# Kernel optimization log

Measured on AMD Instinct MI355X. Metric: run time of the kernel, lower is better.

The kernel has to match this reference:

```python
import jax, jax.numpy as jnp
import numpy as np

E = 2048   # embedding_size
H = 2048   # hidden_size
B = 512    # batch
OUT = 2    # output_size (coords)


def setup_inputs() -> dict:
    key = jax.random.key(0)
    ks = jax.random.split(key, 11)
    s = 0.02
    return {
        "embedding": jax.random.normal(ks[0], (B, E), dtype=jnp.float32),
        "max_seq_length": 256,
        "W_embed": jax.random.normal(ks[1], (H, E), dtype=jnp.float32) * s,
        "b_embed": jnp.zeros((H,), dtype=jnp.float32),
        "W_ih": jax.random.normal(ks[2], (4 * H, OUT), dtype=jnp.float32) * s,
        "b_ih": jnp.zeros((4 * H,), dtype=jnp.float32),
        "W_hh": jax.random.normal(ks[3], (4 * H, H), dtype=jnp.float32) * s,
        "b_hh": jnp.zeros((4 * H,), dtype=jnp.float32),
        "W_out": jax.random.normal(ks[4], (OUT, H), dtype=jnp.float32) * s,
        "b_out": jnp.zeros((OUT,), dtype=jnp.float32),
        "W_stop": jax.random.normal(ks[5], (1, H), dtype=jnp.float32) * s,
        "b_stop": jnp.zeros((1,), dtype=jnp.float32),
    }


def reference(embedding, max_seq_length, W_embed, b_embed, W_ih, b_ih,
              W_hh, b_hh, W_out, b_out, W_stop, b_stop):
    # h_0 from embedding head (num_layers == 1)
    h0 = embedding @ W_embed.T + b_embed          # (B, H)
    c0 = jnp.zeros_like(h0)
    x0 = jnp.zeros((embedding.shape[0], OUT), dtype=embedding.dtype)

    def step(carry, _):
        h, c, x = carry
        gates = x @ W_ih.T + b_ih + h @ W_hh.T + b_hh    # (B, 4H)
        i, f, g, o = jnp.split(gates, 4, axis=-1)         # torch gate order i,f,g,o
        c = jax.nn.sigmoid(f) * c + jax.nn.sigmoid(i) * jnp.tanh(g)
        h = jax.nn.sigmoid(o) * jnp.tanh(c)
        coord = h @ W_out.T + b_out                        # (B, 2)
        stop = jax.nn.sigmoid(h @ W_stop.T + b_stop)       # (B, 1)
        return (h, c, coord), (coord, stop)

    _, (coords, stops) = jax.lax.scan(step, (h0, c0, x0), xs=None,
                                      length=max_seq_length)
    outputs = jnp.transpose(coords, (1, 0, 2))     # (B, T, 2)
    stop_probs = jnp.transpose(stops, (1, 0, 2))   # (B, T, 1)
    return outputs, stop_probs
```

## Files before the change

kernel.cpp:

```cpp
#include <hip/hip_runtime.h>
#include <stdint.h>

#define E_DIM 2048
#define H_DIM 2048
#define B_DIM 512
#define T_DIM 256
#define G4H   8192

typedef unsigned short u16;
typedef __attribute__((ext_vector_type(8))) short bf16x8;
typedef __attribute__((ext_vector_type(4))) float f32x4;

__device__ inline u16 f2b(float f) {
  union { float f; uint32_t i; } v; v.f = f;
  uint32_t u = v.i;
  return (u16)((u + 0x7FFFu + ((u >> 16) & 1u)) >> 16);
}
__device__ inline float b2f(u16 u) {
  union { uint32_t i; float f; } v; v.i = ((uint32_t)u) << 16; return v.f;
}

__global__ __launch_bounds__(256) void convert_bf16(const float* __restrict__ s,
                                                    u16* __restrict__ d, int n4) {
  int i = blockIdx.x * 256 + threadIdx.x;
  if (i < n4) {
    float4 f = ((const float4*)s)[i];
    ushort4 o;
    o.x = f2b(f.x); o.y = f2b(f.y); o.z = f2b(f.z); o.w = f2b(f.w);
    ((ushort4*)d)[i] = o;
  }
}

__global__ __launch_bounds__(256) void build_weff(const float* __restrict__ W,
                                                  const float* __restrict__ W_ih,
                                                  const float* __restrict__ W_out,
                                                  u16* __restrict__ Wz) {
  int id = blockIdx.x * 256 + threadIdx.x;
  int lane = id & 63;
  int k32  = (id >> 6) & 63;
  int n16  = id >> 12;
  int np = n16 * 16 + (lane & 15);
  int k  = k32 * 32 + (lane >> 4) * 8;
  int g = np & 3, jrow = np >> 2;
  int src = g * H_DIM + jrow;
  float wi0 = W_ih[src * 2 + 0], wi1 = W_ih[src * 2 + 1];
  const float* sw = W + (size_t)src * H_DIM + k;
  u16 out[8];
  for (int j = 0; j < 8; ++j) {
    float v = sw[j] + wi0 * W_out[k + j] + wi1 * W_out[H_DIM + k + j];
    out[j] = f2b(v);
  }
  u16* dst = Wz + (size_t)id * 8;
  *(ushort4*)(dst) = *(ushort4*)&out[0];
  *(ushort4*)(dst + 4) = *(ushort4*)&out[4];
}

__global__ __launch_bounds__(256) void build_epi(const float* __restrict__ b_ih,
                                                 const float* __restrict__ b_hh,
                                                 const float* __restrict__ W_ih,
                                                 const float* __restrict__ b_out,
                                                 float* __restrict__ epi) {
  int np = blockIdx.x * 256 + threadIdx.x;
  int src = (np & 3) * H_DIM + (np >> 2);
  float wi0 = W_ih[src * 2 + 0], wi1 = W_ih[src * 2 + 1];
  float4 e;
  e.x = b_ih[src] + b_hh[src] + b_out[0] * wi0 + b_out[1] * wi1;
  e.y = wi0;
  e.z = wi1;
  e.w = 0.f;
  ((float4*)epi)[np] = e;
}

#define BM 64
#define BN 128
#define BK 32
__global__ __launch_bounds__(256) void gemm_bt(const u16* __restrict__ A,
                                               const u16* __restrict__ Bm,
                                               float* __restrict__ C,
                                               int M, int N, int K) {
  __shared__ u16 sA[BM * BK];
  __shared__ u16 sB[BN * BK];
  const int t = threadIdx.x;
  const int bm0 = blockIdx.y * BM, bn0 = blockIdx.x * BN;
  const int wave = t >> 6, lane = t & 63;
  const int wm = (wave >> 1) * 32, wn = (wave & 1) * 64;
  const int r16 = lane & 15, quad = lane >> 4;

  f32x4 acc[2][4];
  const f32x4 z = {0.f, 0.f, 0.f, 0.f};
  for (int i = 0; i < 2; ++i)
    for (int j = 0; j < 4; ++j) acc[i][j] = z;

  const int arow = t >> 2, acg = t & 3;

  for (int k0 = 0; k0 < K; k0 += BK) {
    __syncthreads();
    *(uint4*)&sA[arow * BK + acg * 8] =
        *(const uint4*)&A[(size_t)(bm0 + arow) * K + k0 + acg * 8];
    for (int i = 0; i < 2; ++i) {
      int c = t + 256 * i;
      int row = c >> 2, cg = c & 3;
      *(uint4*)&sB[row * BK + cg * 8] =
          *(const uint4*)&Bm[(size_t)(bn0 + row) * K + k0 + cg * 8];
    }
    __syncthreads();
    bf16x8 af[2], bfr[4];
    for (int mt = 0; mt < 2; ++mt)
      af[mt] = *(const bf16x8*)&sA[(wm + mt * 16 + r16) * BK + quad * 8];
    for (int nt = 0; nt < 4; ++nt)
      bfr[nt] = *(const bf16x8*)&sB[(wn + nt * 16 + r16) * BK + quad * 8];
    for (int mt = 0; mt < 2; ++mt)
      for (int nt = 0; nt < 4; ++nt)
        acc[mt][nt] = __builtin_amdgcn_mfma_f32_16x16x32_bf16(af[mt], bfr[nt],
                                                              acc[mt][nt], 0, 0, 0);
  }
  for (int mt = 0; mt < 2; ++mt)
    for (int nt = 0; nt < 4; ++nt) {
      int row = bm0 + wm + mt * 16 + quad * 4;
      int col = bn0 + wn + nt * 16 + r16;
      for (int r = 0; r < 4; ++r)
        C[(size_t)(row + r) * N + col] = acc[mt][nt][r];
    }
}

__global__ __launch_bounds__(256) void init_state(const float* __restrict__ h0pre,
                                                  const float* __restrict__ b_embed,
                                                  u16* __restrict__ h,
                                                  float* __restrict__ c,
                                                  float* __restrict__ xzero) {
  int idx = blockIdx.x * 256 + threadIdx.x;
  int bg = idx >> 11, k = idx & (H_DIM - 1);
  float v = h0pre[idx] + b_embed[k];
  size_t chunk = (((size_t)(bg >> 4)) * 64 + (k >> 5)) * 64 + ((k >> 3) & 3) * 16 + (bg & 15);
  size_t pos = chunk * 8 + (k & 7);
  h[pos] = f2b(v);
  c[pos] = 0.f;
  if (idx < B_DIM * 2) xzero[idx] = 0.f;
}

__global__ __launch_bounds__(64) void calc_xcorr(const float* __restrict__ h0pre,
                                                 const float* __restrict__ b_embed,
                                                 const float* __restrict__ W_out,
                                                 const float* __restrict__ b_out,
                                                 float* __restrict__ xc) {
  int m = blockIdx.x, ln = threadIdx.x;
  float s0 = 0.f, s1 = 0.f;
  for (int k = ln; k < H_DIM; k += 64) {
    float hv = h0pre[(size_t)m * H_DIM + k] + b_embed[k];
    s0 += hv * W_out[k];
    s1 += hv * W_out[H_DIM + k];
  }
  for (int off = 32; off > 0; off >>= 1) {
    s0 += __shfl_down(s0, off);
    s1 += __shfl_down(s1, off);
  }
  if (ln == 0) {
    xc[m * 2 + 0] = -(s0 + b_out[0]);
    xc[m * 2 + 1] = -(s1 + b_out[1]);
  }
}

__global__ __launch_bounds__(256) void init_out(const float* __restrict__ b_out,
                                                const float* __restrict__ b_stop,
                                                float* __restrict__ coords,
                                                float* __restrict__ stops) {
  int i = blockIdx.x * 256 + threadIdx.x;
  coords[i * 2 + 0] = b_out[0];
  coords[i * 2 + 1] = b_out[1];
  stops[i] = b_stop[0];
}

__global__ __launch_bounds__(256) void finalize_stops(float* __restrict__ stops) {
  int i = blockIdx.x * 256 + threadIdx.x;
  stops[i] = 1.f / (1.f + __expf(-stops[i]));
}

__global__ __launch_bounds__(512) void gemm_lstm(const u16* __restrict__ hA,
                                                 const u16* __restrict__ Wz,
                                                 const float* __restrict__ epi,
                                                 const float* __restrict__ x,
                                                 float* __restrict__ c,
                                                 u16* __restrict__ h_out,
                                                 const float* __restrict__ W_out,
                                                 const float* __restrict__ W_stop,
                                                 float* __restrict__ coords,
                                                 float* __restrict__ stops,
                                                 int trow) {
  __shared__ char smem[131072];
  float* cb = (float*)smem;
  float* gt = (float*)smem;

  const int bid = blockIdx.x;
  const int nt = (bid & 7) * 8 + ((bid >> 3) & 7);
  const int mt = bid >> 6;
  const int bm0 = mt * 128;

  const int t = threadIdx.x, wv = t >> 6, ln = t & 63;
  const int wn2 = wv & 1, kq = wv >> 1;
  const int r16 = ln & 15, quad = ln >> 4;

  const u16* pA[8];
  const u16* pB[4];
  for (int i = 0; i < 8; ++i)
    pA[i] = hA + (size_t)((bm0 >> 4) + i) * 32768 + (size_t)(kq * 16) * 512 + ln * 8;
  for (int i = 0; i < 4; ++i)
    pB[i] = Wz + (size_t)(nt * 8 + wn2 * 4 + i) * 32768 + (size_t)(kq * 16) * 512 + ln * 8;

  f32x4 acc[8][4];
  const f32x4 z = {0.f, 0.f, 0.f, 0.f};
  for (int i = 0; i < 8; ++i)
    for (int j = 0; j < 4; ++j) acc[i][j] = z;

  bf16x8 af[2][8], bf[2][4];
  for (int i = 0; i < 8; ++i) af[0][i] = *(const bf16x8*)(pA[i]);
  for (int i = 0; i < 4; ++i) bf[0][i] = *(const bf16x8*)(pB[i]);

#pragma unroll 2
  for (int kk = 0; kk < 16; ++kk) {
    const int cu = kk & 1;
    if (kk < 15) {
      const int nx = cu ^ 1;
      const size_t off = (size_t)(kk + 1) * 512;
      for (int i = 0; i < 8; ++i) af[nx][i] = *(const bf16x8*)(pA[i] + off);
      for (int i = 0; i < 4; ++i) bf[nx][i] = *(const bf16x8*)(pB[i] + off);
    }
    for (int mi = 0; mi < 8; ++mi)
      for (int ni = 0; ni < 4; ++ni)
        acc[mi][ni] = __builtin_amdgcn_mfma_f32_16x16x32_bf16(af[cu][mi], bf[cu][ni],
                                                              acc[mi][ni], 0, 0, 0);
  }

  if (kq >= 2) {
    float* dst = cb + ((kq - 2) * 2 + wn2) * 8192;
    for (int mi = 0; mi < 8; ++mi)
      for (int ni = 0; ni < 4; ++ni)
        *(f32x4*)&dst[((mi * 4 + ni) * 64 + ln) * 4] = acc[mi][ni];
  }
  __syncthreads();
  if (kq < 2) {
    const float* src = cb + (kq * 2 + wn2) * 8192;
    for (int mi = 0; mi < 8; ++mi)
      for (int ni = 0; ni < 4; ++ni)
        acc[mi][ni] += *(const f32x4*)&src[((mi * 4 + ni) * 64 + ln) * 4];
  }
  __syncthreads();
  if (kq == 1) {
    float* dst = cb + wn2 * 8192;
    for (int mi = 0; mi < 8; ++mi)
      for (int ni = 0; ni < 4; ++ni)
        *(f32x4*)&dst[((mi * 4 + ni) * 64 + ln) * 4] = acc[mi][ni];
  }
  __syncthreads();
  if (kq == 0) {
    const float* src = cb + wn2 * 8192;
    for (int mi = 0; mi < 8; ++mi)
      for (int ni = 0; ni < 4; ++ni)
        acc[mi][ni] += *(const f32x4*)&src[((mi * 4 + ni) * 64 + ln) * 4];
  }

  for (int half = 0; half < 2; ++half) {
    __syncthreads();
    if (wv < 2) {
      for (int mi = 0; mi < 4; ++mi)
        for (int ni = 0; ni < 4; ++ni) {
          int row = mi * 16 + quad * 4;
          int col = wn2 * 64 + ni * 16 + r16;
          f32x4 v = acc[half * 4 + mi][ni];
          for (int r = 0; r < 4; ++r)
            gt[(row + r) * 132 + col] = v[r];
        }
    }
    __syncthreads();
    if ((wv >> 2) == half) {
      const int q = wv & 3;
      const int lrow = q * 16 + r16;
      const int bg = bm0 + half * 64 + lrow;
      const float x0 = x[bg * 2 + 0], x1 = x[bg * 2 + 1];
      const size_t chunk = (((size_t)(bg >> 4)) * 64 + nt) * 64 + ln;
      const int hc0 = nt * 32 + quad * 8;
      float cv[8]; u16 hv[8];
      float s0 = 0.f, s1 = 0.f, s2 = 0.f;
      const float4* epi4 = (const float4*)epi;
      for (int j = 0; j < 8; ++j) {
        int col = quad * 32 + j * 4;
        float4 g4 = *(const float4*)&gt[lrow * 132 + col];
        float4 e0 = epi4[nt * 128 + col + 0];
        float4 e1 = epi4[nt * 128 + col + 1];
        float4 e2 = epi4[nt * 128 + col + 2];
        float4 e3 = epi4[nt * 128 + col + 3];
        float gi = g4.x + e0.x + x0 * e0.y + x1 * e0.z;
        float gf = g4.y + e1.x + x0 * e1.y + x1 * e1.z;
        float gg = g4.z + e2.x + x0 * e2.y + x1 * e2.z;
        float go = g4.w + e3.x + x0 * e3.y + x1 * e3.z;
        float si = 1.f / (1.f + __expf(-gi));
        float sf = 1.f / (1.f + __expf(-gf));
        float so = 1.f / (1.f + __expf(-go));
        float cn = sf * c[chunk * 8 + j] + si * tanhf(gg);
        cv[j] = cn;
        float hf = so * tanhf(cn);
        hv[j] = f2b(hf);
        s0 += hf * W_out[hc0 + j];
        s1 += hf * W_out[H_DIM + hc0 + j];
        s2 += hf * W_stop[hc0 + j];
      }
      *(float4*)&c[chunk * 8 + 0] = *(float4*)&cv[0];
      *(float4*)&c[chunk * 8 + 4] = *(float4*)&cv[4];
      *(ushort4*)&h_out[chunk * 8 + 0] = *(ushort4*)&hv[0];
      *(ushort4*)&h_out[chunk * 8 + 4] = *(ushort4*)&hv[4];
      s0 += __shfl_xor(s0, 16); s1 += __shfl_xor(s1, 16); s2 += __shfl_xor(s2, 16);
      s0 += __shfl_xor(s0, 32); s1 += __shfl_xor(s1, 32); s2 += __shfl_xor(s2, 32);
      if (quad == 0) {
        atomicAdd(&coords[((size_t)bg * T_DIM + trow) * 2 + 0], s0);
        atomicAdd(&coords[((size_t)bg * T_DIM + trow) * 2 + 1], s1);
        atomicAdd(&stops[(size_t)bg * T_DIM + trow], s2);
      }
    }
  }
}

extern "C" void kernel_launch(void* const* d_in, const int* in_sizes, int n_in,
                              void* d_out, int out_size, void* d_ws, size_t ws_size,
                              hipStream_t stream) {
  const float* embedding = (const float*)d_in[0];
  const float* W_embed   = (const float*)d_in[2];
  const float* b_embed   = (const float*)d_in[3];
  const float* W_ih      = (const float*)d_in[4];
  const float* b_ih      = (const float*)d_in[5];
  const float* W_hh      = (const float*)d_in[6];
  const float* b_hh      = (const float*)d_in[7];
  const float* W_out     = (const float*)d_in[8];
  const float* b_out     = (const float*)d_in[9];
  const float* W_stop    = (const float*)d_in[10];
  const float* b_stop    = (const float*)d_in[11];

  float* coords = (float*)d_out;
  float* stops  = (float*)d_out + (size_t)B_DIM * T_DIM * 2;

  char* ws = (char*)d_ws;
  u16* W_z     = (u16*)ws;   ws += (size_t)G4H * H_DIM * 2;
  u16* W_emb_b = (u16*)ws;   ws += (size_t)H_DIM * E_DIM * 2;
  u16* emb_b   = (u16*)ws;   ws += (size_t)B_DIM * E_DIM * 2;
  float* h0pre = (float*)ws; ws += (size_t)B_DIM * H_DIM * 4;
  float* epi   = (float*)ws; ws += (size_t)G4H * 4 * 4;
  float* cbuf  = (float*)ws; ws += (size_t)B_DIM * H_DIM * 4;
  u16* hbuf0   = (u16*)ws;   ws += (size_t)B_DIM * H_DIM * 2;
  u16* hbuf1   = (u16*)ws;   ws += (size_t)B_DIM * H_DIM * 2;
  float* xcorr = (float*)ws; ws += (size_t)B_DIM * 2 * 4;
  float* xzero = (float*)ws; ws += (size_t)B_DIM * 2 * 4;

  convert_bf16<<<(B_DIM * E_DIM / 4 + 255) / 256, 256, 0, stream>>>(embedding, emb_b, B_DIM * E_DIM / 4);
  convert_bf16<<<(H_DIM * E_DIM / 4 + 255) / 256, 256, 0, stream>>>(W_embed, W_emb_b, H_DIM * E_DIM / 4);
  build_weff<<<(G4H * H_DIM / 8) / 256, 256, 0, stream>>>(W_hh, W_ih, W_out, W_z);
  build_epi<<<G4H / 256, 256, 0, stream>>>(b_ih, b_hh, W_ih, b_out, epi);
  init_out<<<(B_DIM * T_DIM) / 256, 256, 0, stream>>>(b_out, b_stop, coords, stops);

  gemm_bt<<<dim3(H_DIM / BN, B_DIM / BM), 256, 0, stream>>>(emb_b, W_emb_b, h0pre,
                                                            B_DIM, H_DIM, E_DIM);
  init_state<<<(B_DIM * H_DIM) / 256, 256, 0, stream>>>(h0pre, b_embed, hbuf0, cbuf, xzero);
  calc_xcorr<<<B_DIM, 64, 0, stream>>>(h0pre, b_embed, W_out, b_out, xcorr);

  for (int t = 0; t < T_DIM; ++t) {
    u16* h_in  = (t & 1) ? hbuf1 : hbuf0;
    u16* h_out = (t & 1) ? hbuf0 : hbuf1;
    const float* xv = (t == 0) ? xcorr : xzero;
    gemm_lstm<<<256, 512, 0, stream>>>(h_in, W_z, epi, xv, cbuf, h_out,
                                       W_out, W_stop, coords, stops, t);
  }
  finalize_stops<<<(B_DIM * T_DIM) / 256, 256, 0, stream>>>(stops);
}
```

Measured before the change: 7.818 ms.

## Switch recurrent GEMM to 32x32x16 MFMA with matching pre-swizzled layouts

Replaces the 16x16x32 bf16 MFMA tiles with 32x32x16 MFMA tiles in the per-step gate GEMM. The weight, hidden-state and cell-state swizzled layouts (build_weff, init_state and the epilogue addressing) are changed to 32-row by 16-k chunks to match. The larger instruction cuts the number of MFMA issues and the operand loads per FLOP in the recurrent kernel. In exchange, the accumulator-to-shared scatter becomes more complex and all layout index math has to stay consistent across kernels.

```diff
diff --git a/kernel.cpp b/kernel.cpp
--- a/kernel.cpp
+++ b/kernel.cpp
@@ -10,6 +10,7 @@
 typedef unsigned short u16;
 typedef __attribute__((ext_vector_type(8))) short bf16x8;
 typedef __attribute__((ext_vector_type(4))) float f32x4;
+typedef __attribute__((ext_vector_type(16))) float f32x16;
 
 __device__ inline u16 f2b(float f) {
   union { float f; uint32_t i; } v; v.f = f;
@@ -37,10 +38,10 @@
                                                   u16* __restrict__ Wz) {
   int id = blockIdx.x * 256 + threadIdx.x;
   int lane = id & 63;
-  int k32  = (id >> 6) & 63;
-  int n16  = id >> 12;
-  int np = n16 * 16 + (lane & 15);
-  int k  = k32 * 32 + (lane >> 4) * 8;
+  int k16  = (id >> 6) & 127;
+  int n32  = id >> 13;
+  int np = n32 * 32 + (lane & 31);
+  int k  = k16 * 16 + (lane >> 5) * 8;
   int g = np & 3, jrow = np >> 2;
   int src = g * H_DIM + jrow;
   float wi0 = W_ih[src * 2 + 0], wi1 = W_ih[src * 2 + 1];
@@ -131,7 +132,7 @@
   int idx = blockIdx.x * 256 + threadIdx.x;
   int bg = idx >> 11, k = idx & (H_DIM - 1);
   float v = h0pre[idx] + b_embed[k];
-  size_t chunk = (((size_t)(bg >> 4)) * 64 + (k >> 5)) * 64 + ((k >> 3) & 3) * 16 + (bg & 15);
+  size_t chunk = (((size_t)(bg >> 5)) * 128 + (k >> 4)) * 64 + ((k >> 3) & 1) * 32 + (bg & 31);
   size_t pos = chunk * 8 + (k & 7);
   h[pos] = f2b(v);
   c[pos] = 0.f;
@@ -199,76 +200,93 @@
   const int wn2 = wv & 1, kq = wv >> 1;
   const int r16 = ln & 15, quad = ln >> 4;
 
-  const u16* pA[8];
-  const u16* pB[4];
-  for (int i = 0; i < 8; ++i)
-    pA[i] = hA + (size_t)((bm0 >> 4) + i) * 32768 + (size_t)(kq * 16) * 512 + ln * 8;
+  const u16* pA[4];
+  const u16* pB[2];
   for (int i = 0; i < 4; ++i)
-    pB[i] = Wz + (size_t)(nt * 8 + wn2 * 4 + i) * 32768 + (size_t)(kq * 16) * 512 + ln * 8;
-
-  f32x4 acc[8][4];
-  const f32x4 z = {0.f, 0.f, 0.f, 0.f};
-  for (int i = 0; i < 8; ++i)
-    for (int j = 0; j < 4; ++j) acc[i][j] = z;
-
-  bf16x8 af[2][8], bf[2][4];
-  for (int i = 0; i < 8; ++i) af[0][i] = *(const bf16x8*)(pA[i]);
-  for (int i = 0; i < 4; ++i) bf[0][i] = *(const bf16x8*)(pB[i]);
+    pA[i] = hA + ((size_t)(mt * 4 + i) * 128 + kq * 32) * 512 + ln * 8;
+  for (int i = 0; i < 2; ++i)
+    pB[i] = Wz + ((size_t)(nt * 4 + wn2 * 2 + i) * 128 + kq * 32) * 512 + ln * 8;
+
+  f32x16 acc[4][2];
+  for (int i = 0; i < 4; ++i)
+    for (int j = 0; j < 2; ++j)
+      for (int r = 0; r < 16; ++r) acc[i][j][r] = 0.f;
+
+  bf16x8 af[2][4], bf[2][2];
+  for (int i = 0; i < 4; ++i) af[0][i] = *(const bf16x8*)(pA[i]);
+  for (int i = 0; i < 2; ++i) bf[0][i] = *(const bf16x8*)(pB[i]);
 
 #pragma unroll 2
-  for (int kk = 0; kk < 16; ++kk) {
+  for (int kk = 0; kk < 32; ++kk) {
     const int cu = kk & 1;
-    if (kk < 15) {
+    if (kk < 31) {
       const int nx = cu ^ 1;
       const size_t off = (size_t)(kk + 1) * 512;
-      for (int i = 0; i < 8; ++i) af[nx][i] = *(const bf16x8*)(pA[i] + off);
-      for (int i = 0; i < 4; ++i) bf[nx][i] = *(const bf16x8*)(pB[i] + off);
-    }
-    for (int mi = 0; mi < 8; ++mi)
-      for (int ni = 0; ni < 4; ++ni)
-        acc[mi][ni] = __builtin_amdgcn_mfma_f32_16x16x32_bf16(af[cu][mi], bf[cu][ni],
+      for (int i = 0; i < 4; ++i) af[nx][i] = *(const bf16x8*)(pA[i] + off);
+      for (int i = 0; i < 2; ++i) bf[nx][i] = *(const bf16x8*)(pB[i] + off);
+    }
+    for (int mi = 0; mi < 4; ++mi)
+      for (int ni = 0; ni < 2; ++ni)
+        acc[mi][ni] = __builtin_amdgcn_mfma_f32_32x32x16_bf16(af[cu][mi], bf[cu][ni],
                                                               acc[mi][ni], 0, 0, 0);
   }
 
   if (kq >= 2) {
     float* dst = cb + ((kq - 2) * 2 + wn2) * 8192;
-    for (int mi = 0; mi < 8; ++mi)
-      for (int ni = 0; ni < 4; ++ni)
-        *(f32x4*)&dst[((mi * 4 + ni) * 64 + ln) * 4] = acc[mi][ni];
+    for (int mi = 0; mi < 4; ++mi)
+      for (int ni = 0; ni < 2; ++ni)
+        for (int q4 = 0; q4 < 4; ++q4) {
+          f32x4 v = {acc[mi][ni][q4 * 4 + 0], acc[mi][ni][q4 * 4 + 1],
+                     acc[mi][ni][q4 * 4 + 2], acc[mi][ni][q4 * 4 + 3]};
+          *(f32x4*)&dst[(((mi * 2 + ni) * 4 + q4) * 64 + ln) * 4] = v;
+        }
   }
   __syncthreads();
   if (kq < 2) {
     const float* src = cb + (kq * 2 + wn2) * 8192;
-    for (int mi = 0; mi < 8; ++mi)
-      for (int ni = 0; ni < 4; ++ni)
-        acc[mi][ni] += *(const f32x4*)&src[((mi * 4 + ni) * 64 + ln) * 4];
+    for (int mi = 0; mi < 4; ++mi)
+      for (int ni = 0; ni < 2; ++ni)
+        for (int q4 = 0; q4 < 4; ++q4) {
+          f32x4 p = *(const f32x4*)&src[(((mi * 2 + ni) * 4 + q4) * 64 + ln) * 4];
+          for (int e = 0; e < 4; ++e) acc[mi][ni][q4 * 4 + e] += p[e];
+        }
   }
   __syncthreads();
   if (kq == 1) {
     float* dst = cb + wn2 * 8192;
-    for (int mi = 0; mi < 8; ++mi)
-      for (int ni = 0; ni < 4; ++ni)
-        *(f32x4*)&dst[((mi * 4 + ni) * 64 + ln) * 4] = acc[mi][ni];
+    for (int mi = 0; mi < 4; ++mi)
+      for (int ni = 0; ni < 2; ++ni)
+        for (int q4 = 0; q4 < 4; ++q4) {
+          f32x4 v = {acc[mi][ni][q4 * 4 + 0], acc[mi][ni][q4 * 4 + 1],
+                     acc[mi][ni][q4 * 4 + 2], acc[mi][ni][q4 * 4 + 3]};
+          *(f32x4*)&dst[(((mi * 2 + ni) * 4 + q4) * 64 + ln) * 4] = v;
+        }
   }
   __syncthreads();
   if (kq == 0) {
     const float* src = cb + wn2 * 8192;
-    for (int mi = 0; mi < 8; ++mi)
-      for (int ni = 0; ni < 4; ++ni)
-        acc[mi][ni] += *(const f32x4*)&src[((mi * 4 + ni) * 64 + ln) * 4];
+    for (int mi = 0; mi < 4; ++mi)
+      for (int ni = 0; ni < 2; ++ni)
+        for (int q4 = 0; q4 < 4; ++q4) {
+          f32x4 p = *(const f32x4*)&src[(((mi * 2 + ni) * 4 + q4) * 64 + ln) * 4];
+          for (int e = 0; e < 4; ++e) acc[mi][ni][q4 * 4 + e] += p[e];
+        }
   }
 
   for (int half = 0; half < 2; ++half) {
     __syncthreads();
     if (wv < 2) {
-      for (int mi = 0; mi < 4; ++mi)
-        for (int ni = 0; ni < 4; ++ni) {
-          int row = mi * 16 + quad * 4;
-          int col = wn2 * 64 + ni * 16 + r16;
-          f32x4 v = acc[half * 4 + mi][ni];
-          for (int r = 0; r < 4; ++r)
-            gt[(row + r) * 132 + col] = v[r];
-        }
+      for (int mi2 = 0; mi2 < 2; ++mi2) {
+        int mi = half * 2 + mi2;
+        for (int ni = 0; ni < 2; ++ni) {
+          int col = wn2 * 64 + ni * 32 + (ln & 31);
+          int rbase = mi2 * 32 + 4 * (ln >> 5);
+          for (int r = 0; r < 16; ++r) {
+            int row = rbase + (r & 3) + 8 * (r >> 2);
+            gt[row * 132 + col] = acc[mi][ni][r];
+          }
+        }
+      }
     }
     __syncthreads();
     if ((wv >> 2) == half) {
@@ -276,8 +294,9 @@
       const int lrow = q * 16 + r16;
       const int bg = bm0 + half * 64 + lrow;
       const float x0 = x[bg * 2 + 0], x1 = x[bg * 2 + 1];
-      const size_t chunk = (((size_t)(bg >> 4)) * 64 + nt) * 64 + ln;
       const int hc0 = nt * 32 + quad * 8;
+      const size_t pos = (((size_t)(bg >> 5)) * 128 + (hc0 >> 4)) * 512 +
+                         ((hc0 >> 3) & 1) * 256 + (bg & 31) * 8;
       float cv[8]; u16 hv[8];
       float s0 = 0.f, s1 = 0.f, s2 = 0.f;
       const float4* epi4 = (const float4*)epi;
@@ -295,7 +314,7 @@
         float si = 1.f / (1.f + __expf(-gi));
         float sf = 1.f / (1.f + __expf(-gf));
         float so = 1.f / (1.f + __expf(-go));
-        float cn = sf * c[chunk * 8 + j] + si * tanhf(gg);
+        float cn = sf * c[pos + j] + si * tanhf(gg);
         cv[j] = cn;
         float hf = so * tanhf(cn);
         hv[j] = f2b(hf);
@@ -303,10 +322,10 @@
         s1 += hf * W_out[H_DIM + hc0 + j];
         s2 += hf * W_stop[hc0 + j];
       }
-      *(float4*)&c[chunk * 8 + 0] = *(float4*)&cv[0];
-      *(float4*)&c[chunk * 8 + 4] = *(float4*)&cv[4];
-      *(ushort4*)&h_out[chunk * 8 + 0] = *(ushort4*)&hv[0];
-      *(ushort4*)&h_out[chunk * 8 + 4] = *(ushort4*)&hv[4];
+      *(float4*)&c[pos + 0] = *(float4*)&cv[0];
+      *(float4*)&c[pos + 4] = *(float4*)&cv[4];
+      *(ushort4*)&h_out[pos + 0] = *(ushort4*)&hv[0];
+      *(ushort4*)&h_out[pos + 4] = *(ushort4*)&hv[4];
       s0 += __shfl_xor(s0, 16); s1 += __shfl_xor(s1, 16); s2 += __shfl_xor(s2, 16);
       s0 += __shfl_xor(s0, 32); s1 += __shfl_xor(s1, 32); s2 += __shfl_xor(s2, 32);
       if (quad == 0) {
```

Result: slower. 8.484 ms (+8.5%).

## Halve LSTM step M-tile to 64 rows and launch 512 blocks

Applied to the files above, without the earlier changes.

The per-step fused GEMM+LSTM kernel now uses 64-row batch tiles instead of 128, doubling the grid to 512 blocks. Shared memory is halved and launch bounds request 4 blocks per CU, so occupancy and CU coverage on the 256-CU device rise. The explicit register double-buffering of A/B fragments is dropped for a simple unroll-1 load-then-MFMA loop. In exchange each block re-reads the weight tile with half the batch reuse, which doubles weight traffic from L2, and the loop no longer overlaps loads with MFMAs in software.

```diff
diff --git a/kernel.cpp b/kernel.cpp
--- a/kernel.cpp
+++ b/kernel.cpp
@@ -175,145 +175,133 @@
   stops[i] = 1.f / (1.f + __expf(-stops[i]));
 }
 
-__global__ __launch_bounds__(512) void gemm_lstm(const u16* __restrict__ hA,
-                                                 const u16* __restrict__ Wz,
-                                                 const float* __restrict__ epi,
-                                                 const float* __restrict__ x,
-                                                 float* __restrict__ c,
-                                                 u16* __restrict__ h_out,
-                                                 const float* __restrict__ W_out,
-                                                 const float* __restrict__ W_stop,
-                                                 float* __restrict__ coords,
-                                                 float* __restrict__ stops,
-                                                 int trow) {
-  __shared__ char smem[131072];
+__global__ __launch_bounds__(512, 4) void gemm_lstm(const u16* __restrict__ hA,
+                                                    const u16* __restrict__ Wz,
+                                                    const float* __restrict__ epi,
+                                                    const float* __restrict__ x,
+                                                    float* __restrict__ c,
+                                                    u16* __restrict__ h_out,
+                                                    const float* __restrict__ W_out,
+                                                    const float* __restrict__ W_stop,
+                                                    float* __restrict__ coords,
+                                                    float* __restrict__ stops,
+                                                    int trow) {
+  __shared__ char smem[65536];
   float* cb = (float*)smem;
   float* gt = (float*)smem;
 
   const int bid = blockIdx.x;
   const int nt = (bid & 7) * 8 + ((bid >> 3) & 7);
   const int mt = bid >> 6;
-  const int bm0 = mt * 128;
+  const int bm0 = mt * 64;
 
   const int t = threadIdx.x, wv = t >> 6, ln = t & 63;
-  const int wn2 = wv & 1, kq = wv >> 1;
+  const int nh = wv & 1, kq = wv >> 1;
   const int r16 = ln & 15, quad = ln >> 4;
 
-  const u16* pA[8];
-  const u16* pB[4];
-  for (int i = 0; i < 8; ++i)
-    pA[i] = hA + (size_t)((bm0 >> 4) + i) * 32768 + (size_t)(kq * 16) * 512 + ln * 8;
+  const u16* pA = hA + ((size_t)(mt * 4) * 64 + (size_t)(kq * 16)) * 512 + ln * 8;
+  const u16* pB = Wz + ((size_t)(nt * 8 + nh * 4) * 64 + (size_t)(kq * 16)) * 512 + ln * 8;
+
+  f32x4 acc[4][4];
+  const f32x4 z = {0.f, 0.f, 0.f, 0.f};
   for (int i = 0; i < 4; ++i)
-    pB[i] = Wz + (size_t)(nt * 8 + wn2 * 4 + i) * 32768 + (size_t)(kq * 16) * 512 + ln * 8;
-
-  f32x4 acc[8][4];
-  const f32x4 z = {0.f, 0.f, 0.f, 0.f};
-  for (int i = 0; i < 8; ++i)
     for (int j = 0; j < 4; ++j) acc[i][j] = z;
 
-  bf16x8 af[2][8], bf[2][4];
-  for (int i = 0; i < 8; ++i) af[0][i] = *(const bf16x8*)(pA[i]);
-  for (int i = 0; i < 4; ++i) bf[0][i] = *(const bf16x8*)(pB[i]);
-
-#pragma unroll 2
+#pragma unroll 1
   for (int kk = 0; kk < 16; ++kk) {
-    const int cu = kk & 1;
-    if (kk < 15) {
-      const int nx = cu ^ 1;
-      const size_t off = (size_t)(kk + 1) * 512;
-      for (int i = 0; i < 8; ++i) af[nx][i] = *(const bf16x8*)(pA[i] + off);
-      for (int i = 0; i < 4; ++i) bf[nx][i] = *(const bf16x8*)(pB[i] + off);
+    bf16x8 af[4], bf[4];
+    for (int i = 0; i < 4; ++i) af[i] = *(const bf16x8*)(pA + (size_t)i * 32768);
+    for (int i = 0; i < 4; ++i) bf[i] = *(const bf16x8*)(pB + (size_t)i * 32768);
+    for (int mi = 0; mi < 4; ++mi)
+      for (int ni = 0; ni < 4; ++ni)
+        acc[mi][ni] = __builtin_amdgcn_mfma_f32_16x16x32_bf16(af[mi], bf[ni],
+                                                              acc[mi][ni], 0, 0, 0);
+    pA += 512;
+    pB += 512;
+  }
+
+  if (kq >= 2) {
+    float* dst = cb + ((kq - 2) * 2 + nh) * 4096;
+    for (int mi = 0; mi < 4; ++mi)
+      for (int ni = 0; ni < 4; ++ni)
+        *(f32x4*)&dst[((mi * 4 + ni) * 64 + ln) * 4] = acc[mi][ni];
+  }
+  __syncthreads();
+  if (kq < 2) {
+    const float* src = cb + (kq * 2 + nh) * 4096;
+    for (int mi = 0; mi < 4; ++mi)
+      for (int ni = 0; ni < 4; ++ni)
+        acc[mi][ni] += *(const f32x4*)&src[((mi * 4 + ni) * 64 + ln) * 4];
+  }
+  __syncthreads();
+  if (kq == 1) {
+    float* dst = cb + nh * 4096;
+    for (int mi = 0; mi < 4; ++mi)
+      for (int ni = 0; ni < 4; ++ni)
+        *(f32x4*)&dst[((mi * 4 + ni) * 64 + ln) * 4] = acc[mi][ni];
+  }
+  __syncthreads();
+  if (kq == 0) {
+    const float* src = cb + nh * 4096;
+    for (int mi = 0; mi < 4; ++mi)
+      for (int ni = 0; ni < 4; ++ni)
+        acc[mi][ni] += *(const f32x4*)&src[((mi * 4 + ni) * 64 + ln) * 4];
+  }
+
+  __syncthreads();
+  if (wv < 2) {
+    for (int mi = 0; mi < 4; ++mi)
+      for (int ni = 0; ni < 4; ++ni) {
+        int row = mi * 16 + quad * 4;
+        int col = nh * 64 + ni * 16 + r16;
+        f32x4 v = acc[mi][ni];
+        for (int r = 0; r < 4; ++r)
+          gt[(row + r) * 132 + col] = v[r];
+      }
+  }
+  __syncthreads();
+  if (wv >= 4) {
+    const int q = wv - 4;
+    const int lrow = q * 16 + r16;
+    const int bg = bm0 + lrow;
+    const float x0 = x[bg * 2 + 0], x1 = x[bg * 2 + 1];
+    const size_t chunk = (((size_t)(bg >> 4)) * 64 + nt) * 64 + ln;
+    const int hc0 = nt * 32 + quad * 8;
+    float cv[8]; u16 hv[8];
+    float s0 = 0.f, s1 = 0.f, s2 = 0.f;
+    const float4* epi4 = (const float4*)epi;
+    for (int j = 0; j < 8; ++j) {
+      int col = quad * 32 + j * 4;
+      float4 g4 = *(const float4*)&gt[lrow * 132 + col];
+      float4 e0 = epi4[nt * 128 + col + 0];
+      float4 e1 = epi4[nt * 128 + col + 1];
+      float4 e2 = epi4[nt * 128 + col + 2];
+      float4 e3 = epi4[nt * 128 + col + 3];
+      float gi = g4.x + e0.x + x0 * e0.y + x1 * e0.z;
+      float gf = g4.y + e1.x + x0 * e1.y + x1 * e1.z;
+      float gg = g4.z + e2.x + x0 * e2.y + x1 * e2.z;
+      float go = g4.w + e3.x + x0 * e3.y + x1 * e3.z;
+      float si = 1.f / (1.f + __expf(-gi));
+      float sf = 1.f / (1.f + __expf(-gf));
+      float so = 1.f / (1.f + __expf(-go));
+      float cn = sf * c[chunk * 8 + j] + si * tanhf(gg);
+      cv[j] = cn;
+      float hf = so * tanhf(cn);
+      hv[j] = f2b(hf);
+      s0 += hf * W_out[hc0 + j];
+      s1 += hf * W_out[H_DIM + hc0 + j];
+      s2 += hf * W_stop[hc0 + j];
     }
-    for (int mi = 0; mi < 8; ++mi)
-      for (int ni = 0; ni < 4; ++ni)
-        acc[mi][ni] = __builtin_amdgcn_mfma_f32_16x16x32_bf16(af[cu][mi], bf[cu][ni],
-                                                              acc[mi][ni], 0, 0, 0);
-  }
-
-  if (kq >= 2) {
-    float* dst = cb + ((kq - 2) * 2 + wn2) * 8192;
-    for (int mi = 0; mi < 8; ++mi)
-      for (int ni = 0; ni < 4; ++ni)
-        *(f32x4*)&dst[((mi * 4 + ni) * 64 + ln) * 4] = acc[mi][ni];
-  }
-  __syncthreads();
-  if (kq < 2) {
-    const float* src = cb + (kq * 2 + wn2) * 8192;
-    for (int mi = 0; mi < 8; ++mi)
-      for (int ni = 0; ni < 4; ++ni)
-        acc[mi][ni] += *(const f32x4*)&src[((mi * 4 + ni) * 64 + ln) * 4];
-  }
-  __syncthreads();
-  if (kq == 1) {
-    float* dst = cb + wn2 * 8192;
-    for (int mi = 0; mi < 8; ++mi)
-      for (int ni = 0; ni < 4; ++ni)
-        *(f32x4*)&dst[((mi * 4 + ni) * 64 + ln) * 4] = acc[mi][ni];
-  }
-  __syncthreads();
-  if (kq == 0) {
-    const float* src = cb + wn2 * 8192;
-    for (int mi = 0; mi < 8; ++mi)
-      for (int ni = 0; ni < 4; ++ni)
-        acc[mi][ni] += *(const f32x4*)&src[((mi * 4 + ni) * 64 + ln) * 4];
-  }
-
-  for (int half = 0; half < 2; ++half) {
-    __syncthreads();
-    if (wv < 2) {
-      for (int mi = 0; mi < 4; ++mi)
-        for (int ni = 0; ni < 4; ++ni) {
-          int row = mi * 16 + quad * 4;
-          int col = wn2 * 64 + ni * 16 + r16;
-          f32x4 v = acc[half * 4 + mi][ni];
-          for (int r = 0; r < 4; ++r)
-            gt[(row + r) * 132 + col] = v[r];
-        }
-    }
-    __syncthreads();
-    if ((wv >> 2) == half) {
-      const int q = wv & 3;
-      const int lrow = q * 16 + r16;
-      const int bg = bm0 + half * 64 + lrow;
-      const float x0 = x[bg * 2 + 0], x1 = x[bg * 2 + 1];
-      const size_t chunk = (((size_t)(bg >> 4)) * 64 + nt) * 64 + ln;
-      const int hc0 = nt * 32 + quad * 8;
-      float cv[8]; u16 hv[8];
-      float s0 = 0.f, s1 = 0.f, s2 = 0.f;
-      const float4* epi4 = (const float4*)epi;
-      for (int j = 0; j < 8; ++j) {
-        int col = quad * 32 + j * 4;
-        float4 g4 = *(const float4*)&gt[lrow * 132 + col];
-        float4 e0 = epi4[nt * 128 + col + 0];
-        float4 e1 = epi4[nt * 128 + col + 1];
-        float4 e2 = epi4[nt * 128 + col + 2];
-        float4 e3 = epi4[nt * 128 + col + 3];
-        float gi = g4.x + e0.x + x0 * e0.y + x1 * e0.z;
-        float gf = g4.y + e1.x + x0 * e1.y + x1 * e1.z;
-        float gg = g4.z + e2.x + x0 * e2.y + x1 * e2.z;
-        float go = g4.w + e3.x + x0 * e3.y + x1 * e3.z;
-        float si = 1.f / (1.f + __expf(-gi));
-        float sf = 1.f / (1.f + __expf(-gf));
-        float so = 1.f / (1.f + __expf(-go));
-        float cn = sf * c[chunk * 8 + j] + si * tanhf(gg);
-        cv[j] = cn;
-        float hf = so * tanhf(cn);
-        hv[j] = f2b(hf);
-        s0 += hf * W_out[hc0 + j];
-        s1 += hf * W_out[H_DIM + hc0 + j];
-        s2 += hf * W_stop[hc0 + j];
-      }
-      *(float4*)&c[chunk * 8 + 0] = *(float4*)&cv[0];
-      *(float4*)&c[chunk * 8 + 4] = *(float4*)&cv[4];
-      *(ushort4*)&h_out[chunk * 8 + 0] = *(ushort4*)&hv[0];
-      *(ushort4*)&h_out[chunk * 8 + 4] = *(ushort4*)&hv[4];
-      s0 += __shfl_xor(s0, 16); s1 += __shfl_xor(s1, 16); s2 += __shfl_xor(s2, 16);
-      s0 += __shfl_xor(s0, 32); s1 += __shfl_xor(s1, 32); s2 += __shfl_xor(s2, 32);
-      if (quad == 0) {
-        atomicAdd(&coords[((size_t)bg * T_DIM + trow) * 2 + 0], s0);
-        atomicAdd(&coords[((size_t)bg * T_DIM + trow) * 2 + 1], s1);
-        atomicAdd(&stops[(size_t)bg * T_DIM + trow], s2);
-      }
+    *(float4*)&c[chunk * 8 + 0] = *(float4*)&cv[0];
+    *(float4*)&c[chunk * 8 + 4] = *(float4*)&cv[4];
+    *(ushort4*)&h_out[chunk * 8 + 0] = *(ushort4*)&hv[0];
+    *(ushort4*)&h_out[chunk * 8 + 4] = *(ushort4*)&hv[4];
+    s0 += __shfl_xor(s0, 16); s1 += __shfl_xor(s1, 16); s2 += __shfl_xor(s2, 16);
+    s0 += __shfl_xor(s0, 32); s1 += __shfl_xor(s1, 32); s2 += __shfl_xor(s2, 32);
+    if (quad == 0) {
+      atomicAdd(&coords[((size_t)bg * T_DIM + trow) * 2 + 0], s0);
+      atomicAdd(&coords[((size_t)bg * T_DIM + trow) * 2 + 1], s1);
+      atomicAdd(&stops[(size_t)bg * T_DIM + trow], s2);
     }
   }
 }
@@ -363,7 +351,7 @@
     u16* h_in  = (t & 1) ? hbuf1 : hbuf0;
     u16* h_out = (t & 1) ? hbuf0 : hbuf1;
     const float* xv = (t == 0) ? xcorr : xzero;
-    gemm_lstm<<<256, 512, 0, stream>>>(h_in, W_z, epi, xv, cbuf, h_out,
+    gemm_lstm<<<512, 512, 0, stream>>>(h_in, W_z, epi, xv, cbuf, h_out,
                                        W_out, W_stop, coords, stops, t);
   }
   finalize_stops<<<(B_DIM * T_DIM) / 256, 256, 0, stream>>>(stops);
```

After: 8.055 ms. 1.03x slower.
